# Optimization experiments

Hardware: AMD Instinct MI355X
Metric: run time of the kernel (lower is better)

The kernel has to match this reference:

```python
import jax, jax.numpy as jnp
import numpy as np
import math

B, D, H, W, C = 1, 16, 56, 56, 256
WD, WH, WW = 2, 7, 7
NH, NP = 8, 4
N = WD * WH * WW          # 98 tokens per window
HD = C // NH
NWIN = (D // WD) * (H // WH) * (W // WW)  # 512


def layernorm(x, g, b, eps=1e-5):
    m = x.mean(-1, keepdims=True)
    v = jnp.mean((x - m) ** 2, -1, keepdims=True)
    return (x - m) * jax.lax.rsqrt(v + eps) * g + b


def _reference_points():
    zz = (jnp.arange(WD, dtype=jnp.float32) + 0.5) / WD
    yy = (jnp.arange(WH, dtype=jnp.float32) + 0.5) / WH
    xx = (jnp.arange(WW, dtype=jnp.float32) + 0.5) / WW
    gz, gy, gx = jnp.meshgrid(zz, yy, xx, indexing='ij')
    return jnp.stack([gx.ravel(), gy.ravel(), gz.ravel()], -1)  # (N, 3) in xyz order


def _trilinear(value, loc):
    # value: (Bn, N, NH, HD); loc: (Bn, N, NH, NP, 3) normalized xyz in [0,1]
    # grid_sample semantics: align_corners=False, zero padding
    Bn = value.shape[0]
    v = value.transpose(0, 2, 1, 3)  # (Bn, NH, S, HD), S == N (window volume)
    px = loc[..., 0] * WW - 0.5
    py = loc[..., 1] * WH - 0.5
    pz = loc[..., 2] * WD - 0.5
    x0, y0, z0 = jnp.floor(px), jnp.floor(py), jnp.floor(pz)
    out = jnp.zeros(loc.shape[:-1] + (HD,), value.dtype)
    for dz in (0, 1):
        for dy in (0, 1):
            for dx in (0, 1):
                xi, yi, zi = x0 + dx, y0 + dy, z0 + dz
                wgt = (1 - jnp.abs(px - xi)) * (1 - jnp.abs(py - yi)) * (1 - jnp.abs(pz - zi))
                valid = ((xi >= 0) & (xi < WW) & (yi >= 0) & (yi < WH) & (zi >= 0) & (zi < WD)).astype(value.dtype)
                idx = (jnp.clip(zi, 0, WD - 1) * (WH * WW) + jnp.clip(yi, 0, WH - 1) * WW
                       + jnp.clip(xi, 0, WW - 1)).astype(jnp.int32)  # (Bn, N, NH, NP)
                idxf = idx.transpose(0, 2, 1, 3).reshape(Bn, NH, N * NP)
                g = jnp.take_along_axis(v, idxf[..., None], axis=2)  # (Bn, NH, N*NP, HD)
                g = g.reshape(Bn, NH, N, NP, HD).transpose(0, 2, 1, 3, 4)
                out = out + g * (wgt * valid)[..., None]
    return out  # (Bn, N, NH, NP, HD)


def setup_inputs():
    key = jax.random.key(0)
    ks = jax.random.split(key, 12)

    def lin(k, fin, fout):
        s = 1.0 / np.sqrt(fin)
        kw, kb = jax.random.split(k)
        return (jax.random.uniform(kw, (fin, fout), jnp.float32, -s, s),
                jax.random.uniform(kb, (fout,), jnp.float32, -s, s))

    val_w, val_b = lin(ks[2], C, C)
    off_w, off_b = lin(ks[3], C, NH * NP * 3)
    aw_w, aw_b = lin(ks[4], C, NH * NP)
    out_w, out_b = lin(ks[5], C, C)
    proj_w, proj_b = lin(ks[6], C, C)
    fc1_w, fc1_b = lin(ks[7], C, 4 * C)
    fc2_w, fc2_b = lin(ks[8], 4 * C, C)
    return dict(
        x=jax.random.normal(ks[0], (B, D, H, W, C), jnp.float32),
        mask=jax.random.uniform(ks[1], (NWIN, N, WD, WH, WW), jnp.float32),
        norm1_g=jnp.ones((C,), jnp.float32), norm1_b=jnp.zeros((C,), jnp.float32),
        val_w=val_w, val_b=val_b, off_w=off_w, off_b=off_b,
        aw_w=aw_w, aw_b=aw_b, out_w=out_w, out_b=out_b,
        anorm_g=jnp.ones((C,), jnp.float32), anorm_b=jnp.zeros((C,), jnp.float32),
        proj_w=proj_w, proj_b=proj_b,
        norm2_g=jnp.ones((C,), jnp.float32), norm2_b=jnp.zeros((C,), jnp.float32),
        fc1_w=fc1_w, fc1_b=fc1_b, fc2_w=fc2_w, fc2_b=fc2_b)


def reference(x, mask, norm1_g, norm1_b, val_w, val_b, off_w, off_b, aw_w, aw_b,
              out_w, out_b, anorm_g, anorm_b, proj_w, proj_b,
              norm2_g, norm2_b, fc1_w, fc1_b, fc2_w, fc2_b):
    shortcut = x
    xn = layernorm(x, norm1_g, norm1_b)
    # window partition (dims divisible by window, shift_size = 0 -> no pad/roll)
    xw = xn.reshape(B, D // WD, WD, H // WH, WH, W // WW, WW, C)
    xw = xw.transpose(0, 1, 3, 5, 2, 4, 6, 7).reshape(-1, N, C)  # (B*NWIN, N, C)
    Bn = B * NWIN
    # --- PositionEmbeddingSine over the per-window mask ---
    z_e = jnp.cumsum(mask, 2) * mask / math.pi
    y_e = jnp.cumsum(mask, 3) * mask / math.pi
    x_e = jnp.cumsum(mask, 4) * mask / math.pi
    emb = mask * (jnp.sin(x_e) + jnp.sin(math.pi * y_e) + z_e)
    emb = emb.reshape(NWIN, N, N)  # flatten(2); N == WD*WH*WW
    diag = jnp.diagonal(emb, axis1=1, axis2=2)  # (NWIN, N)
    q = (xw.reshape(B, NWIN, N, C) + diag[None, :, :, None]).reshape(Bn, N, C)
    # --- MS3DDeformAttn over single level = window ---
    ref = _reference_points()  # (N, 3)
    value = (xw @ val_w + val_b).reshape(Bn, N, NH, HD)
    off = (q @ off_w + off_b).reshape(Bn, N, NH, NP, 3)
    aw = jax.nn.softmax((q @ aw_w + aw_b).reshape(Bn, N, NH, NP), axis=-1)
    loc = ref[None, :, None, None, :] + off / jnp.array([WW, WH, WD], jnp.float32)
    sampled = _trilinear(value, loc)                       # (Bn, N, NH, NP, HD)
    attn = (sampled * aw[..., None]).sum(3).reshape(Bn, N, C) @ out_w + out_b
    # WindowAttention3D epilogue: proj(norm(x + attn))
    xw = layernorm(xw + attn, anorm_g, anorm_b) @ proj_w + proj_b
    # window reverse
    xr = xw.reshape(B, D // WD, H // WH, W // WW, WD, WH, WW, C)
    xr = xr.transpose(0, 1, 4, 2, 5, 3, 6, 7).reshape(B, D, H, W, C)
    x = shortcut + xr
    # MLP branch
    h = layernorm(x, norm2_g, norm2_b)
    h = jax.nn.gelu(h @ fc1_w + fc1_b)
    return x + (h @ fc2_w + fc2_b)
```

## Files before the change

### kernel.cpp

```cpp
#include <hip/hip_runtime.h>
#include <hip/hip_bf16.h>
#include <hip/hip_fp16.h>

#define B2F(x) __bfloat162float(x)
#define F2B(x) __float2bfloat16(x)

typedef __bf16 bf16x8 __attribute__((ext_vector_type(8)));
typedef float floatx4 __attribute__((ext_vector_type(4)));

static constexpr int MROWS = 50176;
static constexpr int CDIM  = 256;

enum { MODE_BF16 = 0, MODE_VALOFFAW = 1, MODE_REVERSE = 3, MODE_ATTN = 6 };

#if defined(__has_builtin)
#if __has_builtin(__builtin_amdgcn_global_load_lds)
#define HAS_GLL 1
#endif
#endif
#ifndef HAS_GLL
#define HAS_GLL 0
#endif


__device__ __forceinline__ void win_decode(int r, int& tok) {
    int w = r / 98, n = r - w * 98;
    int dB = w >> 6, hB = (w >> 3) & 7, wB = w & 7;
    int z = n / 49, n2 = n - z * 49, yy = n2 / 7, xx = n2 - yy * 7;
    tok = ((dB * 2 + z) * 56 + hB * 7 + yy) * 56 + wB * 7 + xx;
}

__device__ __forceinline__ float bf2f(unsigned short u) {
    return __uint_as_float(((unsigned)u) << 16);
}

__device__ __forceinline__ float wave_sum64(float v) {
#pragma unroll
    for (int off = 32; off > 0; off >>= 1) v += __shfl_xor(v, off, 64);
    return v;
}


__global__ __launch_bounds__(256) void fused_pre(
    const float* __restrict__ x, const float* __restrict__ n1g, const float* __restrict__ n1b,
    __hip_bfloat16* __restrict__ xw,
    const float* __restrict__ mask, float* __restrict__ diag, float* __restrict__ csum,
    const float* __restrict__ val_w, const float* __restrict__ off_w,
    const float* __restrict__ aw_w,  const float* __restrict__ out_w,
    const float* __restrict__ proj_w, const float* __restrict__ fc1_w,
    const float* __restrict__ fc2_w,
    __hip_bfloat16* __restrict__ valT, __hip_bfloat16* __restrict__ offawT,
    __hip_bfloat16* __restrict__ outT, __hip_bfloat16* __restrict__ projT,
    __hip_bfloat16* __restrict__ fc1T, __hip_bfloat16* __restrict__ fc2T) {
    const int bid = blockIdx.x;
    const int tid = threadIdx.x;

    if (bid < 2944) {
        const float* src; __hip_bfloat16* dst; int K, N, base;
        if (bid < 256)       { src = val_w;  dst = valT;            K = 256;  N = 256;  base = 0; }
        else if (bid < 352)  { src = off_w;  dst = offawT;          K = 256;  N = 96;   base = 256; }
        else if (bid < 384)  { src = aw_w;   dst = offawT + 96*256; K = 256;  N = 32;   base = 352; }
        else if (bid < 640)  { src = out_w;  dst = outT;            K = 256;  N = 256;  base = 384; }
        else if (bid < 896)  { src = proj_w; dst = projT;           K = 256;  N = 256;  base = 640; }
        else if (bid < 1920) { src = fc1_w;  dst = fc1T;            K = 256;  N = 1024; base = 896; }
        else                 { src = fc2_w;  dst = fc2T;            K = 1024; N = 256;  base = 1920; }
        int i = (bid - base) * 256 + tid;
        if (i >= K * N) return;
        int nn = i / K, kk = i - nn * K;
        dst[(size_t)nn * K + kk] = F2B(src[(size_t)kk * N + nn]);
    } else if (bid < 3140) {
        int r = (bid - 2944) * 256 + tid;
        int n = r % 98;
        int z = n / 49, n2 = n - z * 49, yy = n2 / 7, xx = n2 - yy * 7;
        const float* mb = mask + (size_t)r * 98;
        float m = mb[z * 49 + yy * 7 + xx];
        float sz = 0.f, sy = 0.f, sx = 0.f;
        for (int k = 0; k <= z; ++k)  sz += mb[k * 49 + yy * 7 + xx];
        for (int k = 0; k <= yy; ++k) sy += mb[z * 49 + k * 7 + xx];
        for (int k = 0; k <= xx; ++k) sx += mb[z * 49 + yy * 7 + k];
        const float PI = 3.14159265358979323846f;
        diag[r] = m * (sinf(sx * m / PI) + sinf(sy * m) + sz * m / PI);
    } else if (bid == 3140) {
        if (tid < 96) {
            float s = 0.f;
            for (int k = 0; k < 256; ++k) s += off_w[(size_t)k * 96 + tid];
            csum[tid] = s;
        } else if (tid < 128) {
            int n = tid - 96;
            float s = 0.f;
            for (int k = 0; k < 256; ++k) s += aw_w[(size_t)k * 32 + n];
            csum[tid] = s;
        }
    } else {
        const int lane = tid & 63;
        const int rb = (bid - 3141) * 16 + (tid >> 6) * 4;
        const int c0 = lane * 4;
        float4 v[4];
#pragma unroll
        for (int k = 0; k < 4; ++k) {
            int tok; win_decode(rb + k, tok);
            v[k] = *(const float4*)(x + (size_t)tok * CDIM + c0);
        }
        float4 gg = *(const float4*)(n1g + c0);
        float4 bb = *(const float4*)(n1b + c0);
#pragma unroll
        for (int k = 0; k < 4; ++k) {
            float mean = wave_sum64(v[k].x + v[k].y + v[k].z + v[k].w) * (1.f / 256.f);
            float dx = v[k].x - mean, dy = v[k].y - mean, dz = v[k].z - mean, dw = v[k].w - mean;
            float var = wave_sum64(dx * dx + dy * dy + dz * dz + dw * dw) * (1.f / 256.f);
            float rstd = rsqrtf(var + 1e-5f);
            __hip_bfloat16 ob[4] = { F2B(dx * rstd * gg.x + bb.x), F2B(dy * rstd * gg.y + bb.y),
                                     F2B(dz * rstd * gg.z + bb.z), F2B(dw * rstd * gg.w + bb.w) };
            *(ushort4*)(xw + (size_t)(rb + k) * CDIM + c0) = *(const ushort4*)ob;
        }
    }
}


__global__ __launch_bounds__(256) void ln_a_kernel(
    const __hip_bfloat16* __restrict__ s,
    const float* __restrict__ g, const float* __restrict__ b,
    __hip_bfloat16* a2) {
    const int lane = threadIdx.x & 63;
    const int rb = blockIdx.x * 16 + (threadIdx.x >> 6) * 4;
    const int c0 = lane * 4;
    ushort4 sv[4];
#pragma unroll
    for (int k = 0; k < 4; ++k)
        sv[k] = *(const ushort4*)(s + (size_t)(rb + k) * CDIM + c0);
    float4 gg = *(const float4*)(g + c0);
    float4 bb = *(const float4*)(b + c0);
#pragma unroll
    for (int k = 0; k < 4; ++k) {
        float tx = bf2f(sv[k].x), ty = bf2f(sv[k].y), tz = bf2f(sv[k].z), tw = bf2f(sv[k].w);
        float mean = wave_sum64(tx + ty + tz + tw) * (1.f / 256.f);
        float dx = tx - mean, dy = ty - mean, dz = tz - mean, dw = tw - mean;
        float var = wave_sum64(dx * dx + dy * dy + dz * dz + dw * dw) * (1.f / 256.f);
        float rstd = rsqrtf(var + 1e-5f);
        __hip_bfloat16 ob[4] = { F2B(dx * rstd * gg.x + bb.x), F2B(dy * rstd * gg.y + bb.y),
                                 F2B(dz * rstd * gg.z + bb.z), F2B(dw * rstd * gg.w + bb.w) };
        *(ushort4*)((__hip_bfloat16*)a2 + (size_t)(rb + k) * CDIM + c0) = *(const ushort4*)ob;
    }
}

__global__ __launch_bounds__(256) void ln2_kernel(
    const float* __restrict__ xres,
    const float* __restrict__ g, const float* __restrict__ b,
    __hip_bfloat16* __restrict__ hin) {
    const int lane = threadIdx.x & 63;
    const int rb = blockIdx.x * 16 + (threadIdx.x >> 6) * 4;
    const int c0 = lane * 4;
    float4 v[4];
#pragma unroll
    for (int k = 0; k < 4; ++k)
        v[k] = *(const float4*)(xres + (size_t)(rb + k) * CDIM + c0);
    float4 gg = *(const float4*)(g + c0);
    float4 bb = *(const float4*)(b + c0);
#pragma unroll
    for (int k = 0; k < 4; ++k) {
        float mean = wave_sum64(v[k].x + v[k].y + v[k].z + v[k].w) * (1.f / 256.f);
        float dx = v[k].x - mean, dy = v[k].y - mean, dz = v[k].z - mean, dw = v[k].w - mean;
        float var = wave_sum64(dx * dx + dy * dy + dz * dz + dw * dw) * (1.f / 256.f);
        float rstd = rsqrtf(var + 1e-5f);
        __hip_bfloat16 ob[4] = { F2B(dx * rstd * gg.x + bb.x), F2B(dy * rstd * gg.y + bb.y),
                                 F2B(dz * rstd * gg.z + bb.z), F2B(dw * rstd * gg.w + bb.w) };
        *(ushort4*)(hin + (size_t)(rb + k) * CDIM + c0) = *(const ushort4*)ob;
    }
}


__global__ __launch_bounds__(512, 4) void sample_fused(
    const __half* __restrict__ offaw,
    const __hip_bfloat16* __restrict__ value,
    __hip_bfloat16* __restrict__ ai) {
    __shared__ __align__(16) __hip_bfloat16 vs[98 * 256];
    __shared__ __align__(16) __half os[98 * 128];
    const int tid = threadIdx.x;
    const int w = blockIdx.x;

#if HAS_GLL
    {
        const uint4* vsrc = (const uint4*)(value + (size_t)w * 98 * CDIM);
#pragma unroll
        for (int k = 0; k < 7; ++k) {
            int i = tid + k * 512;
            if (i < 3136)
                __builtin_amdgcn_global_load_lds(
                    (const __attribute__((address_space(1))) void*)(vsrc + i),
                    (__attribute__((address_space(3))) void*)(((uint4*)vs) + i), 16, 0, 0);
        }
        const uint4* osrc = (const uint4*)(offaw + (size_t)w * 98 * 128);
#pragma unroll
        for (int k = 0; k < 4; ++k) {
            int i = tid + k * 512;
            if (i < 1568)
                __builtin_amdgcn_global_load_lds(
                    (const __attribute__((address_space(1))) void*)(osrc + i),
                    (__attribute__((address_space(3))) void*)(((uint4*)os) + i), 16, 0, 0);
        }
    }
#else
    {
        const uint4* vsrc = (const uint4*)(value + (size_t)w * 98 * CDIM);
        uint4* vdst = (uint4*)vs;
        for (int i = tid; i < 3136; i += 512) vdst[i] = vsrc[i];
        const uint4* osrc = (const uint4*)(offaw + (size_t)w * 98 * 128);
        uint4* odst = (uint4*)os;
        for (int i = tid; i < 1568; i += 512) odst[i] = osrc[i];
    }
#endif
    __syncthreads();

    const int lane  = tid & 63;
    const int wave  = tid >> 6;
    const int h     = lane >> 3;
    const int s     = lane & 7;
    const int p     = s >> 1;
    const int jbase = (s & 1) * 4;
    const int boff  = lane * 8;
    const int gbase = lane & ~7;

    for (int r = wave; r < 98; r += 8) {
        int z = r / 49, n2 = r - z * 49, yy = n2 / 7, xx = n2 - yy * 7;
        const __half* orow = os + r * 128;

        float l0 = __half2float(orow[96 + h * 4 + 0]);
        float l1 = __half2float(orow[96 + h * 4 + 1]);
        float l2 = __half2float(orow[96 + h * 4 + 2]);
        float l3 = __half2float(orow[96 + h * 4 + 3]);
        float mx = fmaxf(fmaxf(l0, l1), fmaxf(l2, l3));
        float e0 = __expf(l0 - mx), e1 = __expf(l1 - mx), e2 = __expf(l2 - mx), e3 = __expf(l3 - mx);
        float inv = 1.f / (e0 + e1 + e2 + e3);
        float ep = (p == 0) ? e0 : (p == 1) ? e1 : (p == 2) ? e2 : e3;
        float wp = ep * inv;

        float ox = __half2float(orow[h * 12 + p * 3 + 0]);
        float oy = __half2float(orow[h * 12 + p * 3 + 1]);
        float oz = __half2float(orow[h * 12 + p * 3 + 2]);
        float px = (float)xx + ox, py = (float)yy + oy, pz = (float)z + oz;
        float fx0 = floorf(px), fy0 = floorf(py), fz0 = floorf(pz);
        int ix = (int)fx0, iy = (int)fy0, iz = (int)fz0;
        float fx = px - fx0, fy = py - fy0, fz = pz - fz0;

        uint packed[4];
#pragma unroll
        for (int jj = 0; jj < 4; ++jj) {
            int j = jbase + jj;
            int dzz = j >> 2, dyy = (j >> 1) & 1, dxx = j & 1;
            int zi = iz + dzz, yi = iy + dyy, xi = ix + dxx;
            float wz = dzz ? fz : 1.f - fz;
            float wy = dyy ? fy : 1.f - fy;
            float wxw = dxx ? fx : 1.f - fx;
            bool valid = (zi >= 0) & (zi < 2) & (yi >= 0) & (yi < 7) & (xi >= 0) & (xi < 7);
            float wc = valid ? wp * wz * wy * wxw : 0.f;
            int zc = min(max(zi, 0), 1), yc = min(max(yi, 0), 6), xc = min(max(xi, 0), 6);
            int idx = zc * 49 + yc * 7 + xc;
            packed[jj] = ((uint)(idx * 512) << 16) | (uint)__half_as_ushort(__float2half(wc));
        }

        float a0 = 0.f, a1 = 0.f, a2 = 0.f, a3 = 0.f;
#pragma unroll
        for (int jj = 0; jj < 4; ++jj) {
            uint mine = packed[jj];
#pragma unroll
            for (int sl = 0; sl < 8; ++sl) {
                uint pk = __shfl(mine, gbase + sl, 64);
                float wj = __half2float(__ushort_as_half((unsigned short)(pk & 0xffffu)));
                ushort4 v = *(const ushort4*)((const char*)vs + (pk >> 16) + boff);
                a0 += wj * bf2f(v.x);
                a1 += wj * bf2f(v.y);
                a2 += wj * bf2f(v.z);
                a3 += wj * bf2f(v.w);
            }
        }
        __hip_bfloat16 ob[4] = { F2B(a0), F2B(a1), F2B(a2), F2B(a3) };
        *(ushort4*)(ai + ((size_t)w * 98 + r) * CDIM + lane * 4) = *(const ushort4*)ob;
    }
}


template <int MODE>
__global__ __launch_bounds__(256) void gemm_bt(
    const __hip_bfloat16* __restrict__ A,
    const __hip_bfloat16* __restrict__ Bt,
    const int N, const int K,
    const float* __restrict__ bias0,
    const float* __restrict__ bias1,
    const float* __restrict__ bias2,
    void* C,
    void* extra,
    const void* extra2,
    const float* __restrict__ csum) {
    __shared__ __align__(16) __hip_bfloat16 As[2][128 * 32];
    __shared__ __align__(16) __hip_bfloat16 Bs[2][128 * 32];
    const int tid  = threadIdx.x;
    const int lane = tid & 63;
    const int wave = tid >> 6;
    const int wm = (wave >> 1) * 64;
    const int wn = (wave & 1) * 64;
    const int row0 = blockIdx.x * 128;
    const int col0 = blockIdx.y * 128;
    const int l15 = lane & 15;
    const int quad = lane >> 4;

    floatx4 acc[4][4] = {};

    const int sr = tid >> 2;
    const int sk = (tid & 3) * 8;

    const __hip_bfloat16* Ab = A + (size_t)row0 * K + sr * (size_t)K + sk;
    const __hip_bfloat16* Bb = Bt + (size_t)col0 * K + sr * (size_t)K + sk;
    const size_t half64 = (size_t)64 * K;

    auto stage = [&](int buf, int k0) {
#if HAS_GLL
        __builtin_amdgcn_global_load_lds(
            (const __attribute__((address_space(1))) void*)(Ab + k0),
            (__attribute__((address_space(3))) void*)(&As[buf][sr * 32 + sk]), 16, 0, 0);
        __builtin_amdgcn_global_load_lds(
            (const __attribute__((address_space(1))) void*)(Ab + half64 + k0),
            (__attribute__((address_space(3))) void*)(&As[buf][(sr + 64) * 32 + sk]), 16, 0, 0);
        __builtin_amdgcn_global_load_lds(
            (const __attribute__((address_space(1))) void*)(Bb + k0),
            (__attribute__((address_space(3))) void*)(&Bs[buf][sr * 32 + sk]), 16, 0, 0);
        __builtin_amdgcn_global_load_lds(
            (const __attribute__((address_space(1))) void*)(Bb + half64 + k0),
            (__attribute__((address_space(3))) void*)(&Bs[buf][(sr + 64) * 32 + sk]), 16, 0, 0);
#else
        *reinterpret_cast<uint4*>(&As[buf][sr * 32 + sk]) = *reinterpret_cast<const uint4*>(Ab + k0);
        *reinterpret_cast<uint4*>(&As[buf][(sr + 64) * 32 + sk]) = *reinterpret_cast<const uint4*>(Ab + half64 + k0);
        *reinterpret_cast<uint4*>(&Bs[buf][sr * 32 + sk]) = *reinterpret_cast<const uint4*>(Bb + k0);
        *reinterpret_cast<uint4*>(&Bs[buf][(sr + 64) * 32 + sk]) = *reinterpret_cast<const uint4*>(Bb + half64 + k0);
#endif
    };

    const int nk = K >> 5;
    stage(0, 0);
    for (int t = 0; t < nk; ++t) {
        __syncthreads();
        if (t + 1 < nk) stage((t + 1) & 1, (t + 1) * 32);
        const __hip_bfloat16* Asb = As[t & 1];
        const __hip_bfloat16* Bsb = Bs[t & 1];
        bf16x8 af[4], bfg[4];
#pragma unroll
        for (int i = 0; i < 4; ++i)
            af[i] = *reinterpret_cast<const bf16x8*>(&Asb[(wm + i * 16 + l15) * 32 + quad * 8]);
#pragma unroll
        for (int j = 0; j < 4; ++j)
            bfg[j] = *reinterpret_cast<const bf16x8*>(&Bsb[(wn + j * 16 + l15) * 32 + quad * 8]);
#pragma unroll
        for (int i = 0; i < 4; ++i)
#pragma unroll
            for (int j = 0; j < 4; ++j)
                acc[i][j] = __builtin_amdgcn_mfma_f32_16x16x32_bf16(af[i], bfg[j], acc[i][j], 0, 0, 0);
    }

#pragma unroll
    for (int i = 0; i < 4; ++i) {
#pragma unroll
        for (int j = 0; j < 4; ++j) {
#pragma unroll
            for (int rr = 0; rr < 4; ++rr) {
                int row = row0 + wm + i * 16 + quad * 4 + rr;
                int col = col0 + wn + j * 16 + l15;
                float v = acc[i][j][rr];
                if constexpr (MODE == MODE_BF16) {
                    v += bias0[col];
                    ((__hip_bfloat16*)C)[(size_t)row * N + col] = F2B(v);
                } else if constexpr (MODE == MODE_ATTN) {
                    v += bias0[col];
                    const __hip_bfloat16* xwp = (const __hip_bfloat16*)extra2;
                    v += B2F(xwp[(size_t)row * 256 + col]);
                    ((__hip_bfloat16*)C)[(size_t)row * N + col] = F2B(v);
                } else if constexpr (MODE == MODE_VALOFFAW) {
                    if (col < 256) {
                        v += bias0[col];
                        ((__hip_bfloat16*)C)[(size_t)row * 256 + col] = F2B(v);
                    } else {
                        int c2 = col - 256;
                        const float* diag = (const float*)extra2;
                        v += (c2 < 96 ? bias1[c2] : bias2[c2 - 96]);
                        v += diag[row] * csum[c2];
                        ((__half*)extra)[(size_t)row * 128 + c2] = __float2half(v);
                    }
                } else if constexpr (MODE == MODE_REVERSE) {
                    v += bias0[col];
                    int tok; win_decode(row, tok);
                    const float* xin = (const float*)extra2;
                    ((float*)C)[(size_t)tok * CDIM + col] = xin[(size_t)tok * CDIM + col] + v;
                }
            }
        }
    }
}


__global__ __launch_bounds__(512, 4) void mlp_fused(
    const __hip_bfloat16* __restrict__ hin,
    const __hip_bfloat16* __restrict__ fc1T,
    const __hip_bfloat16* __restrict__ fc2T,
    const float* __restrict__ fc1_b, const float* __restrict__ fc2_b,
    float* __restrict__ out) {
    __shared__ __align__(16) __hip_bfloat16 hs[8 * 128 * 32];
    __shared__ __align__(16) __hip_bfloat16 as[2 * 128 * 32];
    const int tid  = threadIdx.x;
    const int lane = tid & 63;
    const int w    = tid >> 6;
    const int r0   = blockIdx.x * 128;
    const int l15  = lane & 15;
    const int quad = lane >> 4;
    const int wm   = (w >> 2) * 64;
    const int wn   = (w & 3) * 64;
    const int ac   = (w & 3) * 16;

    {
        const int row = tid >> 2, ke = (tid & 3) * 8;
#if HAS_GLL
#pragma unroll
        for (int kt = 0; kt < 8; ++kt)
            __builtin_amdgcn_global_load_lds(
                (const __attribute__((address_space(1))) void*)(hin + (size_t)(r0 + row) * 256 + kt * 32 + ke),
                (__attribute__((address_space(3))) void*)(&hs[kt * 4096 + row * 32 + ke]), 16, 0, 0);
#else
#pragma unroll
        for (int kt = 0; kt < 8; ++kt)
            *(uint4*)(&hs[kt * 4096 + row * 32 + ke]) =
                *(const uint4*)(hin + (size_t)(r0 + row) * 256 + kt * 32 + ke);
#endif
    }
    floatx4 acc[4][4] = {};
    const int kt2 = (ac + l15) >> 5, ko = (ac + l15) & 31;
    __syncthreads();

    for (int kk = 0; kk < 1024; kk += 64) {
        floatx4 pa[4] = {};
#pragma unroll
        for (int ks = 0; ks < 8; ++ks) {
            bf16x8 b1 = *(const bf16x8*)(fc1T + (size_t)(kk + ac + l15) * 256 + ks * 32 + quad * 8);
#pragma unroll
            for (int i = 0; i < 4; ++i) {
                bf16x8 a = *(const bf16x8*)(&hs[ks * 4096 + (wm + i * 16 + l15) * 32 + quad * 8]);
                pa[i] = __builtin_amdgcn_mfma_f32_16x16x32_bf16(a, b1, pa[i], 0, 0, 0);
            }
        }
        float bb = fc1_b[kk + ac + l15];
        __syncthreads();
#pragma unroll
        for (int i = 0; i < 4; ++i) {
#pragma unroll
            for (int rr = 0; rr < 4; ++rr) {
                float v = pa[i][rr] + bb;
                float t2 = 1.5957691216057308f * (v + 0.044715f * v * v * v);
                v = v / (1.f + __expf(-t2));
                int row = wm + i * 16 + quad * 4 + rr;
                as[kt2 * 4096 + row * 32 + ko] = F2B(v);
            }
        }
        __syncthreads();
#pragma unroll
        for (int ks = 0; ks < 2; ++ks) {
            bf16x8 a4[4];
#pragma unroll
            for (int i = 0; i < 4; ++i)
                a4[i] = *(const bf16x8*)(&as[ks * 4096 + (wm + i * 16 + l15) * 32 + quad * 8]);
#pragma unroll
            for (int j = 0; j < 4; ++j) {
                bf16x8 b2 = *(const bf16x8*)(fc2T + (size_t)(wn + j * 16 + l15) * 1024 + kk + ks * 32 + quad * 8);
#pragma unroll
                for (int i = 0; i < 4; ++i)
                    acc[i][j] = __builtin_amdgcn_mfma_f32_16x16x32_bf16(a4[i], b2, acc[i][j], 0, 0, 0);
            }
        }
    }
#pragma unroll
    for (int i = 0; i < 4; ++i)
#pragma unroll
        for (int j = 0; j < 4; ++j)
#pragma unroll
            for (int rr = 0; rr < 4; ++rr) {
                int row = r0 + wm + i * 16 + quad * 4 + rr;
                int col = wn + j * 16 + l15;
                out[(size_t)row * 256 + col] += acc[i][j][rr] + fc2_b[col];
            }
}


extern "C" void kernel_launch(void* const* d_in, const int* in_sizes, int n_in,
                              void* d_out, int out_size, void* d_ws, size_t ws_size,
                              hipStream_t stream) {
    const float* x      = (const float*)d_in[0];
    const float* mask   = (const float*)d_in[1];
    const float* n1g    = (const float*)d_in[2];
    const float* n1b    = (const float*)d_in[3];
    const float* val_w  = (const float*)d_in[4];
    const float* val_b  = (const float*)d_in[5];
    const float* off_w  = (const float*)d_in[6];
    const float* off_b  = (const float*)d_in[7];
    const float* aw_w   = (const float*)d_in[8];
    const float* aw_b   = (const float*)d_in[9];
    const float* out_w  = (const float*)d_in[10];
    const float* out_b  = (const float*)d_in[11];
    const float* ang    = (const float*)d_in[12];
    const float* anb    = (const float*)d_in[13];
    const float* proj_w = (const float*)d_in[14];
    const float* proj_b = (const float*)d_in[15];
    const float* n2g    = (const float*)d_in[16];
    const float* n2b    = (const float*)d_in[17];
    const float* fc1_w  = (const float*)d_in[18];
    const float* fc1_b  = (const float*)d_in[19];
    const float* fc2_w  = (const float*)d_in[20];
    const float* fc2_b  = (const float*)d_in[21];

    char* ws = (char*)d_ws;
    size_t o = 0;
    auto alloc = [&](size_t bytes) {
        size_t r = o;
        o += (bytes + 255) & ~(size_t)255;
        return r;
    };
    const size_t M = MROWS;
    const size_t REGION_B = M * 128 * 2 + M * 256 * 2;

    __hip_bfloat16* valT    = (__hip_bfloat16*)(ws + alloc(256 * 256 * 2));
    __hip_bfloat16* offawT  = (__hip_bfloat16*)(ws + alloc(128 * 256 * 2));
    __hip_bfloat16* outT    = (__hip_bfloat16*)(ws + alloc(256 * 256 * 2));
    __hip_bfloat16* projT   = (__hip_bfloat16*)(ws + alloc(256 * 256 * 2));
    __hip_bfloat16* fc1T    = (__hip_bfloat16*)(ws + alloc(1024 * 256 * 2));
    __hip_bfloat16* fc2T    = (__hip_bfloat16*)(ws + alloc(256 * 1024 * 2));
    float*          csum    = (float*)(ws + alloc(128 * 4));
    float*          diag    = (float*)(ws + alloc(M * 4));
    char*           slab1   = ws + alloc(M * 256 * 2);
    char*           region  = ws + alloc(REGION_B);
    (void)ws_size; (void)in_sizes; (void)n_in; (void)out_size;

    __hip_bfloat16* xw    = (__hip_bfloat16*)slab1;
    __hip_bfloat16* a2    = (__hip_bfloat16*)slab1;
    __hip_bfloat16* hin   = (__hip_bfloat16*)slab1;
    __half*         offaw = (__half*)region;
    __hip_bfloat16* ai    = (__hip_bfloat16*)(region + M * 128 * 2);
    __hip_bfloat16* value = (__hip_bfloat16*)d_out;
    __hip_bfloat16* attn  = (__hip_bfloat16*)d_out;
    float*          xres  = (float*)d_out;

    dim3 blk(256);
    hipLaunchKernelGGL(fused_pre, dim3(2944 + 196 + 1 + MROWS / 16), blk, 0, stream,
                       x, n1g, n1b, xw, mask, diag, csum,
                       val_w, off_w, aw_w, out_w, proj_w, fc1_w, fc2_w,
                       valT, offawT, outT, projT, fc1T, fc2T);
    hipLaunchKernelGGL((gemm_bt<MODE_VALOFFAW>), dim3(MROWS / 128, 3), blk, 0, stream,
                       xw, valT, 384, 256, val_b, off_b, aw_b,
                       (void*)value, (void*)offaw, (const void*)diag, csum);
    hipLaunchKernelGGL(sample_fused, dim3(MROWS / 98), dim3(512), 0, stream,
                       offaw, value, ai);
    hipLaunchKernelGGL((gemm_bt<MODE_ATTN>), dim3(MROWS / 128, 2), blk, 0, stream,
                       ai, outT, 256, 256, out_b, (const float*)nullptr, (const float*)nullptr,
                       (void*)attn, (void*)nullptr, (const void*)xw, (const float*)nullptr);
    hipLaunchKernelGGL(ln_a_kernel, dim3(MROWS / 16), blk, 0, stream, attn, ang, anb, a2);
    hipLaunchKernelGGL((gemm_bt<MODE_REVERSE>), dim3(MROWS / 128, 2), blk, 0, stream,
                       a2, projT, 256, 256, proj_b, (const float*)nullptr, (const float*)nullptr,
                       (void*)xres, (void*)nullptr, (const void*)x, (const float*)nullptr);
    hipLaunchKernelGGL(ln2_kernel, dim3(MROWS / 16), blk, 0, stream, xres, n2g, n2b, hin);
    hipLaunchKernelGGL(mlp_fused, dim3(MROWS / 128), dim3(512), 0, stream,
                       hin, fc1T, fc2T, fc1_b, fc2_b, (float*)d_out);
}
```

Before: 486.5 us.

## Fuse both post-attention LayerNorms into full-row GEMM epilogues

Adds a gemm_row_ln kernel in which each block computes a full 128x256 output tile. Row mean and variance come from shuffle reductions plus a small LDS cross-wave reduction, so LayerNorm is applied in the GEMM epilogue. It replaces the out-projection GEMM plus ln_a_kernel and the proj GEMM (with window reverse) plus ln2_kernel, so the intermediate attn and xres rows no longer have to be re-read and two launches go away. The cost is one-pass E[x^2]-mean^2 variance, which is less numerically robust, and fewer, larger blocks per GEMM.

```diff
diff --git a/kernel.cpp b/kernel.cpp
--- a/kernel.cpp
+++ b/kernel.cpp
@@ -11,7 +11,7 @@
 static constexpr int MROWS = 50176;
 static constexpr int CDIM  = 256;
 
-enum { MODE_BF16 = 0, MODE_VALOFFAW = 1, MODE_REVERSE = 3, MODE_ATTN = 6 };
+enum { MODE_BF16 = 0, MODE_VALOFFAW = 1 };
 
 #if defined(__has_builtin)
 #if __has_builtin(__builtin_amdgcn_global_load_lds)
@@ -117,58 +117,6 @@
 }
 
 
-__global__ __launch_bounds__(256) void ln_a_kernel(
-    const __hip_bfloat16* __restrict__ s,
-    const float* __restrict__ g, const float* __restrict__ b,
-    __hip_bfloat16* a2) {
-    const int lane = threadIdx.x & 63;
-    const int rb = blockIdx.x * 16 + (threadIdx.x >> 6) * 4;
-    const int c0 = lane * 4;
-    ushort4 sv[4];
-#pragma unroll
-    for (int k = 0; k < 4; ++k)
-        sv[k] = *(const ushort4*)(s + (size_t)(rb + k) * CDIM + c0);
-    float4 gg = *(const float4*)(g + c0);
-    float4 bb = *(const float4*)(b + c0);
-#pragma unroll
-    for (int k = 0; k < 4; ++k) {
-        float tx = bf2f(sv[k].x), ty = bf2f(sv[k].y), tz = bf2f(sv[k].z), tw = bf2f(sv[k].w);
-        float mean = wave_sum64(tx + ty + tz + tw) * (1.f / 256.f);
-        float dx = tx - mean, dy = ty - mean, dz = tz - mean, dw = tw - mean;
-        float var = wave_sum64(dx * dx + dy * dy + dz * dz + dw * dw) * (1.f / 256.f);
-        float rstd = rsqrtf(var + 1e-5f);
-        __hip_bfloat16 ob[4] = { F2B(dx * rstd * gg.x + bb.x), F2B(dy * rstd * gg.y + bb.y),
-                                 F2B(dz * rstd * gg.z + bb.z), F2B(dw * rstd * gg.w + bb.w) };
-        *(ushort4*)((__hip_bfloat16*)a2 + (size_t)(rb + k) * CDIM + c0) = *(const ushort4*)ob;
-    }
-}
-
-__global__ __launch_bounds__(256) void ln2_kernel(
-    const float* __restrict__ xres,
-    const float* __restrict__ g, const float* __restrict__ b,
-    __hip_bfloat16* __restrict__ hin) {
-    const int lane = threadIdx.x & 63;
-    const int rb = blockIdx.x * 16 + (threadIdx.x >> 6) * 4;
-    const int c0 = lane * 4;
-    float4 v[4];
-#pragma unroll
-    for (int k = 0; k < 4; ++k)
-        v[k] = *(const float4*)(xres + (size_t)(rb + k) * CDIM + c0);
-    float4 gg = *(const float4*)(g + c0);
-    float4 bb = *(const float4*)(b + c0);
-#pragma unroll
-    for (int k = 0; k < 4; ++k) {
-        float mean = wave_sum64(v[k].x + v[k].y + v[k].z + v[k].w) * (1.f / 256.f);
-        float dx = v[k].x - mean, dy = v[k].y - mean, dz = v[k].z - mean, dw = v[k].w - mean;
-        float var = wave_sum64(dx * dx + dy * dy + dz * dz + dw * dw) * (1.f / 256.f);
-        float rstd = rsqrtf(var + 1e-5f);
-        __hip_bfloat16 ob[4] = { F2B(dx * rstd * gg.x + bb.x), F2B(dy * rstd * gg.y + bb.y),
-                                 F2B(dz * rstd * gg.z + bb.z), F2B(dw * rstd * gg.w + bb.w) };
-        *(ushort4*)(hin + (size_t)(rb + k) * CDIM + c0) = *(const ushort4*)ob;
-    }
-}
-
-
 __global__ __launch_bounds__(512, 4) void sample_fused(
     const __half* __restrict__ offaw,
     const __hip_bfloat16* __restrict__ value,
@@ -367,12 +315,7 @@
                 if constexpr (MODE == MODE_BF16) {
                     v += bias0[col];
                     ((__hip_bfloat16*)C)[(size_t)row * N + col] = F2B(v);
-                } else if constexpr (MODE == MODE_ATTN) {
-                    v += bias0[col];
-                    const __hip_bfloat16* xwp = (const __hip_bfloat16*)extra2;
-                    v += B2F(xwp[(size_t)row * 256 + col]);
-                    ((__hip_bfloat16*)C)[(size_t)row * N + col] = F2B(v);
-                } else if constexpr (MODE == MODE_VALOFFAW) {
+                } else {
                     if (col < 256) {
                         v += bias0[col];
                         ((__hip_bfloat16*)C)[(size_t)row * 256 + col] = F2B(v);
@@ -383,12 +326,145 @@
                         v += diag[row] * csum[c2];
                         ((__half*)extra)[(size_t)row * 128 + c2] = __float2half(v);
                     }
-                } else if constexpr (MODE == MODE_REVERSE) {
-                    v += bias0[col];
-                    int tok; win_decode(row, tok);
-                    const float* xin = (const float*)extra2;
-                    ((float*)C)[(size_t)tok * CDIM + col] = xin[(size_t)tok * CDIM + col] + v;
                 }
+            }
+        }
+    }
+}
+
+
+template <int REV>
+__global__ __launch_bounds__(512, 4) void gemm_row_ln(
+    const __hip_bfloat16* __restrict__ A,
+    const __hip_bfloat16* __restrict__ Bt,
+    const float* __restrict__ bias,
+    const __hip_bfloat16* __restrict__ xw,
+    const float* __restrict__ xf,
+    const float* __restrict__ g, const float* __restrict__ b,
+    __hip_bfloat16* __restrict__ obf,
+    float* __restrict__ of32) {
+    __shared__ __align__(16) __hip_bfloat16 As[2][128 * 32];
+    __shared__ __align__(16) __hip_bfloat16 Bs[2][256 * 32];
+    __shared__ float p1[128 * 4], p2[128 * 4];
+    const int tid  = threadIdx.x;
+    const int lane = tid & 63;
+    const int w    = tid >> 6;
+    const int l15  = lane & 15;
+    const int quad = lane >> 4;
+    const int wm   = (w >> 2) * 64;
+    const int wn   = (w & 3) * 64;
+    const int wc   = w & 3;
+    const int row0 = blockIdx.x * 128;
+
+    const int sr = tid >> 2;
+    const int sk = (tid & 3) * 8;
+    const __hip_bfloat16* Ab = A + (size_t)(row0 + sr) * 256 + sk;
+    const __hip_bfloat16* Bb = Bt + (size_t)sr * 256 + sk;
+
+    floatx4 acc[4][4] = {};
+
+    auto stage = [&](int buf, int k0) {
+#if HAS_GLL
+        __builtin_amdgcn_global_load_lds(
+            (const __attribute__((address_space(1))) void*)(Ab + k0),
+            (__attribute__((address_space(3))) void*)(&As[buf][sr * 32 + sk]), 16, 0, 0);
+        __builtin_amdgcn_global_load_lds(
+            (const __attribute__((address_space(1))) void*)(Bb + k0),
+            (__attribute__((address_space(3))) void*)(&Bs[buf][sr * 32 + sk]), 16, 0, 0);
+        __builtin_amdgcn_global_load_lds(
+            (const __attribute__((address_space(1))) void*)(Bb + (size_t)128 * 256 + k0),
+            (__attribute__((address_space(3))) void*)(&Bs[buf][(sr + 128) * 32 + sk]), 16, 0, 0);
+#else
+        *reinterpret_cast<uint4*>(&As[buf][sr * 32 + sk]) = *reinterpret_cast<const uint4*>(Ab + k0);
+        *reinterpret_cast<uint4*>(&Bs[buf][sr * 32 + sk]) = *reinterpret_cast<const uint4*>(Bb + k0);
+        *reinterpret_cast<uint4*>(&Bs[buf][(sr + 128) * 32 + sk]) = *reinterpret_cast<const uint4*>(Bb + (size_t)128 * 256 + k0);
+#endif
+    };
+
+    stage(0, 0);
+    for (int t = 0; t < 8; ++t) {
+        __syncthreads();
+        if (t + 1 < 8) stage((t + 1) & 1, (t + 1) * 32);
+        const __hip_bfloat16* Asb = As[t & 1];
+        const __hip_bfloat16* Bsb = Bs[t & 1];
+        bf16x8 af[4], bfg[4];
+#pragma unroll
+        for (int i = 0; i < 4; ++i)
+            af[i] = *reinterpret_cast<const bf16x8*>(&Asb[(wm + i * 16 + l15) * 32 + quad * 8]);
+#pragma unroll
+        for (int j = 0; j < 4; ++j)
+            bfg[j] = *reinterpret_cast<const bf16x8*>(&Bsb[(wn + j * 16 + l15) * 32 + quad * 8]);
+#pragma unroll
+        for (int i = 0; i < 4; ++i)
+#pragma unroll
+            for (int j = 0; j < 4; ++j)
+                acc[i][j] = __builtin_amdgcn_mfma_f32_16x16x32_bf16(af[i], bfg[j], acc[i][j], 0, 0, 0);
+    }
+
+    float biasj[4], gj[4], bj[4];
+#pragma unroll
+    for (int j = 0; j < 4; ++j) {
+        int col = wn + j * 16 + l15;
+        biasj[j] = bias[col];
+        gj[j] = g[col];
+        bj[j] = b[col];
+    }
+
+#pragma unroll
+    for (int i = 0; i < 4; ++i) {
+#pragma unroll
+        for (int rr = 0; rr < 4; ++rr) {
+            int lrow = wm + i * 16 + quad * 4 + rr;
+            int grow = row0 + lrow;
+            int tok = 0;
+            if (REV) win_decode(grow, tok);
+            float s1 = 0.f, s2 = 0.f;
+#pragma unroll
+            for (int j = 0; j < 4; ++j) {
+                int col = wn + j * 16 + l15;
+                float v = acc[i][j][rr] + biasj[j];
+                if constexpr (REV == 0) {
+                    v += B2F(xw[(size_t)grow * 256 + col]);
+                } else {
+                    v += xf[(size_t)tok * 256 + col];
+                    of32[(size_t)tok * 256 + col] = v;
+                }
+                acc[i][j][rr] = v;
+                s1 += v;
+                s2 += v * v;
+            }
+#pragma unroll
+            for (int off = 1; off < 16; off <<= 1) {
+                s1 += __shfl_xor(s1, off, 64);
+                s2 += __shfl_xor(s2, off, 64);
+            }
+            if (l15 == 0) {
+                p1[lrow * 4 + wc] = s1;
+                p2[lrow * 4 + wc] = s2;
+            }
+        }
+    }
+    __syncthreads();
+
+#pragma unroll
+    for (int i = 0; i < 4; ++i) {
+#pragma unroll
+        for (int rr = 0; rr < 4; ++rr) {
+            int lrow = wm + i * 16 + quad * 4 + rr;
+            int grow = row0 + lrow;
+            int tok = 0;
+            if (REV) win_decode(grow, tok);
+            float t1 = p1[lrow * 4 + 0] + p1[lrow * 4 + 1] + p1[lrow * 4 + 2] + p1[lrow * 4 + 3];
+            float t2 = p2[lrow * 4 + 0] + p2[lrow * 4 + 1] + p2[lrow * 4 + 2] + p2[lrow * 4 + 3];
+            float mean = t1 * (1.f / 256.f);
+            float var = t2 * (1.f / 256.f) - mean * mean;
+            float rstd = rsqrtf(var + 1e-5f);
+            size_t orow = REV ? (size_t)tok : (size_t)grow;
+#pragma unroll
+            for (int j = 0; j < 4; ++j) {
+                int col = wn + j * 16 + l15;
+                float o = (acc[i][j][rr] - mean) * rstd * gj[j] + bj[j];
+                obf[orow * 256 + col] = F2B(o);
             }
         }
     }
@@ -535,11 +611,10 @@
 
     __hip_bfloat16* xw    = (__hip_bfloat16*)slab1;
     __hip_bfloat16* a2    = (__hip_bfloat16*)slab1;
-    __hip_bfloat16* hin   = (__hip_bfloat16*)slab1;
     __half*         offaw = (__half*)region;
     __hip_bfloat16* ai    = (__hip_bfloat16*)(region + M * 128 * 2);
+    __hip_bfloat16* hin   = (__hip_bfloat16*)region;
     __hip_bfloat16* value = (__hip_bfloat16*)d_out;
-    __hip_bfloat16* attn  = (__hip_bfloat16*)d_out;
     float*          xres  = (float*)d_out;
 
     dim3 blk(256);
@@ -552,14 +627,12 @@
                        (void*)value, (void*)offaw, (const void*)diag, csum);
     hipLaunchKernelGGL(sample_fused, dim3(MROWS / 98), dim3(512), 0, stream,
                        offaw, value, ai);
-    hipLaunchKernelGGL((gemm_bt<MODE_ATTN>), dim3(MROWS / 128, 2), blk, 0, stream,
-                       ai, outT, 256, 256, out_b, (const float*)nullptr, (const float*)nullptr,
-                       (void*)attn, (void*)nullptr, (const void*)xw, (const float*)nullptr);
-    hipLaunchKernelGGL(ln_a_kernel, dim3(MROWS / 16), blk, 0, stream, attn, ang, anb, a2);
-    hipLaunchKernelGGL((gemm_bt<MODE_REVERSE>), dim3(MROWS / 128, 2), blk, 0, stream,
-                       a2, projT, 256, 256, proj_b, (const float*)nullptr, (const float*)nullptr,
-                       (void*)xres, (void*)nullptr, (const void*)x, (const float*)nullptr);
-    hipLaunchKernelGGL(ln2_kernel, dim3(MROWS / 16), blk, 0, stream, xres, n2g, n2b, hin);
+    hipLaunchKernelGGL((gemm_row_ln<0>), dim3(MROWS / 128), dim3(512), 0, stream,
+                       ai, outT, out_b, xw, (const float*)nullptr, ang, anb,
+                       a2, (float*)nullptr);
+    hipLaunchKernelGGL((gemm_row_ln<1>), dim3(MROWS / 128), dim3(512), 0, stream,
+                       a2, projT, proj_b, (const __hip_bfloat16*)nullptr, x, n2g, n2b,
+                       hin, xres);
     hipLaunchKernelGGL(mlp_fused, dim3(MROWS / 128), dim3(512), 0, stream,
                        hin, fc1T, fc2T, fc1_b, fc2_b, (float*)d_out);
 }
```

Result: faster. 451.6 us (-7.2%).
